# Kernel optimization log

Measured on AMD Instinct MI355X. Metric: run time of the kernel, lower is better.

## Reference

```python
import jax, jax.numpy as jnp
import numpy as np

N, M, E = 128, 256, 64
S, B = 1024, 512


def setup_inputs() -> dict:
    key = jax.random.key(0)
    ks = jax.random.split(key, 8)
    context = jax.random.normal(ks[0], (S, B, N), dtype=jnp.float32)
    z = jax.random.normal(ks[1], (M, B), dtype=jnp.float32)
    noise = jax.random.normal(ks[2], (N, B), dtype=jnp.float32)
    # parameters (match torch init semantics)
    conv_w = jax.random.normal(ks[3], (N, N, 2), dtype=jnp.float32) * (1.0 / np.sqrt(N * 2))
    conv_b = jnp.zeros((N,), dtype=jnp.float32)
    D = jnp.zeros((N, M), dtype=jnp.float32).at[:, :N].set(jnp.eye(N, dtype=jnp.float32))
    sigma = jnp.ones((N,), dtype=jnp.float32) * 0.05
    temp1 = jnp.array([0.1], dtype=jnp.float32)
    temp2 = jnp.array([0.1], dtype=jnp.float32)
    W1 = jax.random.normal(ks[4], (E, M + N), dtype=jnp.float32) * (1.0 / np.sqrt(M + N))
    b1 = jnp.zeros((E,), dtype=jnp.float32)
    W2 = jax.random.normal(ks[5], (E, E), dtype=jnp.float32) * (1.0 / np.sqrt(E))
    b2 = jnp.zeros((E,), dtype=jnp.float32)
    return {"context": context, "z": z, "noise": noise, "conv_w": conv_w,
            "conv_b": conv_b, "D": D, "sigma": sigma, "temp1": temp1,
            "W1": W1, "b1": b1, "W2": W2, "b2": b2, "temp2": temp2}


def reference(context, z, noise, conv_w, conv_b, D, sigma, temp1, W1, b1, W2, b2, temp2):
    # z_obs = D @ detach(z)  -> [N, B]
    z_obs = D @ jax.lax.stop_gradient(z)
    z_current = z_obs + sigma[:, None] * noise            # [N, B]
    z_current_t = z_current.T                             # [B, N]
    # L1 distance attention over the first S-1 frames
    distances = jnp.sum(jnp.abs(context[:-1] - z_current_t[None]), axis=2)  # [S-1, B]
    attn = jax.nn.softmax(-distances / jnp.abs(temp1[0]), axis=0)           # [S-1, B]
    # conv1d over seq axis: x [B, N, S], w [N_out, N_in, 2], valid padding -> [B, N, S-1]
    x = jnp.transpose(context, (1, 2, 0))
    enc = jax.lax.conv_general_dilated(x, conv_w, window_strides=(1,), padding='VALID',
                                       dimension_numbers=('NCH', 'OIH', 'NCH'))
    enc = enc + conv_b[None, :, None]
    encoded = jnp.transpose(enc, (2, 0, 1))               # [S-1, B, N]
    # attention-weighted sum over frames
    embedding = jnp.einsum('sbn,sb->nb', encoded, attn)   # [N, B]
    combined_t = jnp.concatenate([embedding, z], axis=0).T  # [B, N+M]
    h = jax.nn.relu(combined_t @ W1.T + b1)
    mlp_out = h @ W2.T + b2                               # [B, E]
    w_exp = jax.nn.softmax(-mlp_out.T / jnp.abs(temp2[0]), axis=0)  # [E, B]
    return w_exp
```

## Files before the change

kernel.cpp:

```cpp
#include <hip/hip_runtime.h>
#include <math.h>

#define Bq 512
#define Nq 128
#define Mq 256
#define Eq 64
#define SM1 1023
#define LOG2E 1.4426950408889634f

__device__ __forceinline__ float waveReduceSumAll(float x) {
    x += __int_as_float(__builtin_amdgcn_update_dpp(0, __float_as_int(x), 0x111, 0xf, 0xf, true));
    x += __int_as_float(__builtin_amdgcn_update_dpp(0, __float_as_int(x), 0x112, 0xf, 0xf, true));
    x += __int_as_float(__builtin_amdgcn_update_dpp(0, __float_as_int(x), 0x114, 0xf, 0xf, true));
    x += __int_as_float(__builtin_amdgcn_update_dpp(0, __float_as_int(x), 0x118, 0xf, 0xf, true));
    x += __int_as_float(__builtin_amdgcn_update_dpp(0, __float_as_int(x), 0x142, 0xf, 0xf, true));
    x += __int_as_float(__builtin_amdgcn_update_dpp(0, __float_as_int(x), 0x143, 0xf, 0xf, true));
    return __int_as_float(__builtin_amdgcn_readlane(__float_as_int(x), 63));
}

#define ROW_BODY(K, RK, DOLOAD)                                          \
    {                                                                    \
        float2 c  = buf[(K)];                                            \
        float2 cn = buf[((K) + 1) & 7];                                  \
        if (DOLOAD) buf[(K)] = p2[(size_t)min((RK) + 8, hi) * 32768];    \
        float d = fabsf(c.x - zcx) + fabsf(c.y - zcy);                   \
        d = waveReduceSumAll(d);                                         \
        float v = d * negt;                    \
        float mnew = fmaxf(mrun, v);                                     \
        float sc = exp2f(mrun - mnew);           \
        float w  = exp2f(v - mnew);                                      \
        mrun = mnew;                                                     \
        Zrun = fmaf(Zrun, sc, w);                                        \
        a0x = fmaf(a0x, sc, w * c.x);                                    \
        a0y = fmaf(a0y, sc, w * c.y);                                    \
        a1x = fmaf(a1x, sc, w * cn.x);                                   \
        a1y = fmaf(a1y, sc, w * cn.y);                                   \
    }

extern "C" __global__ void __launch_bounds__(512, 4)
gating_kernel(const float* __restrict__ context,
              const float* __restrict__ z,
              const float* __restrict__ noise,
              const float* __restrict__ conv_w,
              const float* __restrict__ conv_b,
              const float* __restrict__ D,
              const float* __restrict__ sigma,
              const float* __restrict__ temp1,
              const float* __restrict__ W1,
              const float* __restrict__ b1,
              const float* __restrict__ W2,
              const float* __restrict__ b2,
              const float* __restrict__ temp2,
              float* __restrict__ out)
{
    const int b    = blockIdx.x;
    const int tid  = threadIdx.x;
    const int wave = tid >> 6;
    const int lane = tid & 63;

    __shared__ __align__(16) float sA0[8][128];
    __shared__ __align__(16) float sA1[8][128];
    __shared__ float smx[8];
    __shared__ float sZ[8];
    __shared__ __align__(16) float gA0[128];
    __shared__ __align__(16) float gA1[128];
    __shared__ __align__(16) float semb[128];
    __shared__ __align__(16) float szc[128];
    __shared__ __align__(16) float szcol[256];
    __shared__ __align__(16) float shb[64];

    const int lo = wave * 128;
    const int hi = min(SM1, lo + 128);
    const float2* p2 = (const float2*)context + (size_t)b * 64 + lane;

    float2 buf[8];
    #pragma unroll
    for (int j = 0; j < 8; ++j)
        buf[j] = p2[(size_t)min(lo + j, hi) * 32768];

    if (tid < 256) szcol[tid] = z[tid * Bq + b];
    __syncthreads();
    if (tid < 128) {
        const float4* Drow = (const float4*)(D + tid * Mq);
        float acc0 = 0.f, acc1 = 0.f, acc2 = 0.f, acc3 = 0.f;
        #pragma unroll 8
        for (int i = 0; i < 64; ++i) {
            float4 dv = Drow[i];
            acc0 = fmaf(dv.x, szcol[4 * i + 0], acc0);
            acc1 = fmaf(dv.y, szcol[4 * i + 1], acc1);
            acc2 = fmaf(dv.z, szcol[4 * i + 2], acc2);
            acc3 = fmaf(dv.w, szcol[4 * i + 3], acc3);
        }
        szc[tid] = (acc0 + acc1) + (acc2 + acc3) + sigma[tid] * noise[tid * Bq + b];
    }
    __syncthreads();

    const float negt = -LOG2E / fabsf(temp1[0]);
    const float zcx = szc[2 * lane];
    const float zcy = szc[2 * lane + 1];

    float mrun = -INFINITY, Zrun = 0.f;
    float a0x = 0.f, a0y = 0.f, a1x = 0.f, a1y = 0.f;

    int r = lo;
    for (; r + 8 <= hi; r += 8) {
        #pragma unroll
        for (int k = 0; k < 8; ++k)
            ROW_BODY(k, r + k, 1)
    }
    #pragma unroll
    for (int j = 0; j < 7; ++j) {
        if (r + j < hi)
            ROW_BODY(j, r + j, 0)
    }

    *(float2*)&sA0[wave][2 * lane] = make_float2(a0x, a0y);
    *(float2*)&sA1[wave][2 * lane] = make_float2(a1x, a1y);
    if (lane == 0) { smx[wave] = mrun; sZ[wave] = Zrun; }
    __syncthreads();

    float gm = smx[0];
    #pragma unroll
    for (int k = 1; k < 8; ++k) gm = fmaxf(gm, smx[k]);
    float scl[8];
    float Gz = 0.f;
    #pragma unroll
    for (int k = 0; k < 8; ++k) { scl[k] = exp2f(smx[k] - gm); Gz = fmaf(scl[k], sZ[k], Gz); }

    if (tid < 128) {
        float acc = 0.f;
        #pragma unroll
        for (int k = 0; k < 8; ++k) acc = fmaf(scl[k], sA0[k][tid], acc);
        gA0[tid] = acc;
    } else if (tid < 256) {
        const int t = tid - 128;
        float acc = 0.f;
        #pragma unroll
        for (int k = 0; k < 8; ++k) acc = fmaf(scl[k], sA1[k][t], acc);
        gA1[t] = acc;
    }
    __syncthreads();

    if (tid < 128) {
        const float4* wr = (const float4*)(conv_w + tid * 256);
        float acc = 0.f;
        #pragma unroll 8
        for (int i = 0; i < 64; ++i) {
            float4 w4 = wr[i];
            acc = fmaf(w4.x, gA0[2 * i], acc);
            acc = fmaf(w4.y, gA1[2 * i], acc);
            acc = fmaf(w4.z, gA0[2 * i + 1], acc);
            acc = fmaf(w4.w, gA1[2 * i + 1], acc);
        }
        semb[tid] = acc / Gz + conv_b[tid];
    }
    __syncthreads();

    if (tid < 64) {
        const float* w1r = W1 + tid * (Nq + Mq);
        float acc = b1[tid];
        #pragma unroll 8
        for (int i = 0; i < 128; ++i) acc = fmaf(w1r[i], semb[i], acc);
        #pragma unroll 8
        for (int i = 0; i < 256; ++i) acc = fmaf(w1r[128 + i], szcol[i], acc);
        shb[tid] = fmaxf(acc, 0.f);
    }
    __syncthreads();

    if (tid < 64) {
        const float* w2r = W2 + tid * Eq;
        float acc = b2[tid];
        #pragma unroll 8
        for (int j = 0; j < 64; ++j) acc = fmaf(w2r[j], shb[j], acc);
        float v = -acc * (LOG2E / fabsf(temp2[0]));
        float mx = v;
        #pragma unroll
        for (int off = 32; off > 0; off >>= 1) mx = fmaxf(mx, __shfl_xor(mx, off, 64));
        float w = exp2f(v - mx);
        float s = w;
        #pragma unroll
        for (int off = 32; off > 0; off >>= 1) s += __shfl_xor(s, off, 64);
        out[tid * Bq + b] = w / s;
    }
}

extern "C" void kernel_launch(void* const* d_in, const int* in_sizes, int n_in,
                              void* d_out, int out_size, void* d_ws, size_t ws_size,
                              hipStream_t stream) {
    const float* context = (const float*)d_in[0];
    const float* z       = (const float*)d_in[1];
    const float* noise   = (const float*)d_in[2];
    const float* conv_w  = (const float*)d_in[3];
    const float* conv_b  = (const float*)d_in[4];
    const float* D       = (const float*)d_in[5];
    const float* sigma   = (const float*)d_in[6];
    const float* temp1   = (const float*)d_in[7];
    const float* W1      = (const float*)d_in[8];
    const float* b1      = (const float*)d_in[9];
    const float* W2      = (const float*)d_in[10];
    const float* b2      = (const float*)d_in[11];
    const float* temp2   = (const float*)d_in[12];
    float* out = (float*)d_out;

    gating_kernel<<<dim3(Bq), dim3(512), 0, stream>>>(
        context, z, noise, conv_w, conv_b, D, sigma, temp1,
        W1, b1, W2, b2, temp2, out);
}
```

Baseline: 69.87 us.

## Split gating kernel into zc, sequence-split streaming, and merge kernels

Splits the single fused kernel into three launches. A small kernel computes z_current for all columns. A streaming kernel runs 1024 blocks, each handling two batch columns over a quarter of the sequence: half-waves, float4 loads and 16-deep register prefetch, writing partial online-softmax results to workspace. A merge kernel combines the four partials and runs the conv/MLP/softmax tail with vectorized W1 loads. The aim is more parallelism and wider memory accesses on the 268MB context stream, at the cost of extra launches and workspace traffic.

New measurement: 128.0 us. +83.2%, slower.

```diff
diff --git a/kernel.cpp b/kernel.cpp
--- a/kernel.cpp
+++ b/kernel.cpp
@@ -8,141 +8,198 @@
 #define SM1 1023
 #define LOG2E 1.4426950408889634f
 
-__device__ __forceinline__ float waveReduceSumAll(float x) {
-    x += __int_as_float(__builtin_amdgcn_update_dpp(0, __float_as_int(x), 0x111, 0xf, 0xf, true));
-    x += __int_as_float(__builtin_amdgcn_update_dpp(0, __float_as_int(x), 0x112, 0xf, 0xf, true));
-    x += __int_as_float(__builtin_amdgcn_update_dpp(0, __float_as_int(x), 0x114, 0xf, 0xf, true));
-    x += __int_as_float(__builtin_amdgcn_update_dpp(0, __float_as_int(x), 0x118, 0xf, 0xf, true));
-    x += __int_as_float(__builtin_amdgcn_update_dpp(0, __float_as_int(x), 0x142, 0xf, 0xf, true));
-    x += __int_as_float(__builtin_amdgcn_update_dpp(0, __float_as_int(x), 0x143, 0xf, 0xf, true));
-    return __int_as_float(__builtin_amdgcn_readlane(__float_as_int(x), 63));
-}
-
-#define ROW_BODY(K, RK, DOLOAD)                                          \
+#define WS_ZC 0
+#define WS_A0 65536
+#define WS_A1 327680
+#define WS_MZ 589824
+
+__device__ __forceinline__ float halfReduce32(float x) {
+    x += __int_as_float(__builtin_amdgcn_update_dpp(0, __float_as_int(x), 0x0B1, 0xf, 0xf, true));
+    x += __int_as_float(__builtin_amdgcn_update_dpp(0, __float_as_int(x), 0x04E, 0xf, 0xf, true));
+    x += __int_as_float(__builtin_amdgcn_update_dpp(0, __float_as_int(x), 0x141, 0xf, 0xf, true));
+    x += __int_as_float(__builtin_amdgcn_update_dpp(0, __float_as_int(x), 0x140, 0xf, 0xf, true));
+    x += __int_as_float(__builtin_amdgcn_ds_swizzle(__float_as_int(x), 0x401F));
+    return x;
+}
+
+extern "C" __global__ void __launch_bounds__(512)
+zc_kernel(const float* __restrict__ z, const float* __restrict__ noise,
+          const float* __restrict__ D, const float* __restrict__ sigma,
+          float* __restrict__ ws)
+{
+    const int b4 = blockIdx.x * 4;
+    const int t  = threadIdx.x;
+    __shared__ float zs[4][256];
+    for (int i = t; i < 1024; i += 512)
+        zs[i >> 8][i & 255] = z[(i & 255) * Bq + b4 + (i >> 8)];
+    __syncthreads();
+    const int c = t >> 7, o = t & 127;
+    const float4* Dr = (const float4*)(D + o * Mq);
+    const float* zc = zs[c];
+    float a0 = 0.f, a1 = 0.f, a2 = 0.f, a3 = 0.f;
+    #pragma unroll 8
+    for (int i = 0; i < 64; ++i) {
+        float4 dv = Dr[i];
+        a0 = fmaf(dv.x, zc[4 * i + 0], a0);
+        a1 = fmaf(dv.y, zc[4 * i + 1], a1);
+        a2 = fmaf(dv.z, zc[4 * i + 2], a2);
+        a3 = fmaf(dv.w, zc[4 * i + 3], a3);
+    }
+    ws[WS_ZC + (b4 + c) * Nq + o] =
+        (a0 + a1) + (a2 + a3) + sigma[o] * noise[o * Bq + b4 + c];
+}
+
+#define ROW_BODY(K, RK, DOREFILL, CN)                                    \
     {                                                                    \
-        float2 c  = buf[(K)];                                            \
-        float2 cn = buf[((K) + 1) & 7];                                  \
-        if (DOLOAD) buf[(K)] = p2[(size_t)min((RK) + 8, hi) * 32768];    \
-        float d = fabsf(c.x - zcx) + fabsf(c.y - zcy);                   \
-        d = waveReduceSumAll(d);                                         \
-        float v = d * negt;                    \
+        float4 c  = buf[(K)];                                            \
+        float4 cn = (CN);                                                \
+        if (DOREFILL) buf[(K)] = p4[(size_t)((RK) + 16) * 16384];        \
+        float d = (fabsf(c.x - zcv.x) + fabsf(c.y - zcv.y)) +            \
+                  (fabsf(c.z - zcv.z) + fabsf(c.w - zcv.w));             \
+        d = halfReduce32(d);                                             \
+        float v = d * negt;                                              \
         float mnew = fmaxf(mrun, v);                                     \
-        float sc = exp2f(mrun - mnew);           \
+        float sc = exp2f(mrun - mnew);                                   \
         float w  = exp2f(v - mnew);                                      \
         mrun = mnew;                                                     \
         Zrun = fmaf(Zrun, sc, w);                                        \
-        a0x = fmaf(a0x, sc, w * c.x);                                    \
-        a0y = fmaf(a0y, sc, w * c.y);                                    \
-        a1x = fmaf(a1x, sc, w * cn.x);                                   \
-        a1y = fmaf(a1y, sc, w * cn.y);                                   \
-    }
-
-extern "C" __global__ void __launch_bounds__(512, 4)
-gating_kernel(const float* __restrict__ context,
-              const float* __restrict__ z,
-              const float* __restrict__ noise,
-              const float* __restrict__ conv_w,
-              const float* __restrict__ conv_b,
-              const float* __restrict__ D,
-              const float* __restrict__ sigma,
+        a0.x = fmaf(a0.x, sc, w * c.x);                                  \
+        a0.y = fmaf(a0.y, sc, w * c.y);                                  \
+        a0.z = fmaf(a0.z, sc, w * c.z);                                  \
+        a0.w = fmaf(a0.w, sc, w * c.w);                                  \
+        a1.x = fmaf(a1.x, sc, w * cn.x);                                 \
+        a1.y = fmaf(a1.y, sc, w * cn.y);                                 \
+        a1.z = fmaf(a1.z, sc, w * cn.z);                                 \
+        a1.w = fmaf(a1.w, sc, w * cn.w);                                 \
+    }
+
+extern "C" __global__ void __launch_bounds__(512, 8)
+stream_kernel(const float* __restrict__ context,
               const float* __restrict__ temp1,
-              const float* __restrict__ W1,
-              const float* __restrict__ b1,
-              const float* __restrict__ W2,
-              const float* __restrict__ b2,
-              const float* __restrict__ temp2,
-              float* __restrict__ out)
+              float* __restrict__ ws)
 {
-    const int b    = blockIdx.x;
     const int tid  = threadIdx.x;
     const int wave = tid >> 6;
     const int lane = tid & 63;
-
-    __shared__ __align__(16) float sA0[8][128];
-    __shared__ __align__(16) float sA1[8][128];
-    __shared__ float smx[8];
-    __shared__ float sZ[8];
+    const int half = lane >> 5;
+    const int l5   = lane & 31;
+    const int q    = blockIdx.x & 3;
+    const int b0   = (blockIdx.x >> 2) * 2;
+
+    __shared__ __align__(16) float sA0[8][2][128];
+    __shared__ __align__(16) float sA1[8][2][128];
+    __shared__ float sM[8][2];
+    __shared__ float sZw[8][2];
+
+    const int lo = q * 256 + wave * 32;
+    const int hi = min(SM1, lo + 32);
+
+    const float4* p4 = (const float4*)context + (size_t)b0 * 32 + lane;
+
+    float4 buf[16];
+    #pragma unroll
+    for (int j = 0; j < 16; ++j)
+        buf[j] = p4[(size_t)(lo + j) * 16384];
+    float4 cextra = p4[(size_t)hi * 16384];
+
+    const float4 zcv = *(const float4*)(ws + WS_ZC + (size_t)(b0 + half) * Nq + l5 * 4);
+    const float negt = -LOG2E / fabsf(temp1[0]);
+
+    float mrun = -INFINITY, Zrun = 0.f;
+    float4 a0 = make_float4(0.f, 0.f, 0.f, 0.f);
+    float4 a1 = make_float4(0.f, 0.f, 0.f, 0.f);
+
+    #pragma unroll
+    for (int k = 0; k < 16; ++k)
+        ROW_BODY(k, lo + k, 1, buf[(k + 1) & 15])
+    #pragma unroll
+    for (int j = 0; j < 15; ++j) {
+        if (lo + 16 + j < hi)
+            ROW_BODY(j, lo + 16 + j, 0, buf[j + 1])
+    }
+    if (lo + 31 < hi)
+        ROW_BODY(15, lo + 31, 0, cextra)
+
+    *(float4*)&sA0[wave][half][l5 * 4] = a0;
+    *(float4*)&sA1[wave][half][l5 * 4] = a1;
+    if (l5 == 0) { sM[wave][half] = mrun; sZw[wave][half] = Zrun; }
+    __syncthreads();
+
+    const int c = (tid >> 7) & 1;
+    const int o = tid & 127;
+    float gm = sM[0][c];
+    #pragma unroll
+    for (int w = 1; w < 8; ++w) gm = fmaxf(gm, sM[w][c]);
+    float scl[8];
+    float Gz = 0.f;
+    #pragma unroll
+    for (int w = 0; w < 8; ++w) { scl[w] = exp2f(sM[w][c] - gm); Gz = fmaf(scl[w], sZw[w][c], Gz); }
+
+    const size_t pslot = (size_t)q * Bq + b0 + c;
+    if (tid < 256) {
+        float acc = 0.f;
+        #pragma unroll
+        for (int w = 0; w < 8; ++w) acc = fmaf(scl[w], sA0[w][c][o], acc);
+        ws[WS_A0 + pslot * Nq + o] = acc;
+        if (o == 0) {
+            ws[WS_MZ + pslot * 2]     = gm;
+            ws[WS_MZ + pslot * 2 + 1] = Gz;
+        }
+    } else {
+        float acc = 0.f;
+        #pragma unroll
+        for (int w = 0; w < 8; ++w) acc = fmaf(scl[w], sA1[w][c][o], acc);
+        ws[WS_A1 + pslot * Nq + o] = acc;
+    }
+}
+
+extern "C" __global__ void __launch_bounds__(128)
+merge_kernel(const float* __restrict__ ws,
+             const float* __restrict__ z,
+             const float* __restrict__ conv_w,
+             const float* __restrict__ conv_b,
+             const float* __restrict__ W1,
+             const float* __restrict__ b1,
+             const float* __restrict__ W2,
+             const float* __restrict__ b2,
+             const float* __restrict__ temp2,
+             float* __restrict__ out)
+{
+    const int col = blockIdx.x;
+    const int t   = threadIdx.x;
     __shared__ __align__(16) float gA0[128];
     __shared__ __align__(16) float gA1[128];
     __shared__ __align__(16) float semb[128];
-    __shared__ __align__(16) float szc[128];
     __shared__ __align__(16) float szcol[256];
     __shared__ __align__(16) float shb[64];
 
-    const int lo = wave * 128;
-    const int hi = min(SM1, lo + 128);
-    const float2* p2 = (const float2*)context + (size_t)b * 64 + lane;
-
-    float2 buf[8];
-    #pragma unroll
-    for (int j = 0; j < 8; ++j)
-        buf[j] = p2[(size_t)min(lo + j, hi) * 32768];
-
-    if (tid < 256) szcol[tid] = z[tid * Bq + b];
-    __syncthreads();
-    if (tid < 128) {
-        const float4* Drow = (const float4*)(D + tid * Mq);
-        float acc0 = 0.f, acc1 = 0.f, acc2 = 0.f, acc3 = 0.f;
-        #pragma unroll 8
-        for (int i = 0; i < 64; ++i) {
-            float4 dv = Drow[i];
-            acc0 = fmaf(dv.x, szcol[4 * i + 0], acc0);
-            acc1 = fmaf(dv.y, szcol[4 * i + 1], acc1);
-            acc2 = fmaf(dv.z, szcol[4 * i + 2], acc2);
-            acc3 = fmaf(dv.w, szcol[4 * i + 3], acc3);
-        }
-        szc[tid] = (acc0 + acc1) + (acc2 + acc3) + sigma[tid] * noise[tid * Bq + b];
-    }
-    __syncthreads();
-
-    const float negt = -LOG2E / fabsf(temp1[0]);
-    const float zcx = szc[2 * lane];
-    const float zcy = szc[2 * lane + 1];
-
-    float mrun = -INFINITY, Zrun = 0.f;
-    float a0x = 0.f, a0y = 0.f, a1x = 0.f, a1y = 0.f;
-
-    int r = lo;
-    for (; r + 8 <= hi; r += 8) {
-        #pragma unroll
-        for (int k = 0; k < 8; ++k)
-            ROW_BODY(k, r + k, 1)
-    }
-    #pragma unroll
-    for (int j = 0; j < 7; ++j) {
-        if (r + j < hi)
-            ROW_BODY(j, r + j, 0)
-    }
-
-    *(float2*)&sA0[wave][2 * lane] = make_float2(a0x, a0y);
-    *(float2*)&sA1[wave][2 * lane] = make_float2(a1x, a1y);
-    if (lane == 0) { smx[wave] = mrun; sZ[wave] = Zrun; }
-    __syncthreads();
-
-    float gm = smx[0];
-    #pragma unroll
-    for (int k = 1; k < 8; ++k) gm = fmaxf(gm, smx[k]);
-    float scl[8];
+    szcol[t]       = z[t * Bq + col];
+    szcol[t + 128] = z[(t + 128) * Bq + col];
+
+    float m[4], Zp[4];
+    #pragma unroll
+    for (int p = 0; p < 4; ++p) {
+        m[p]  = ws[WS_MZ + ((size_t)p * Bq + col) * 2];
+        Zp[p] = ws[WS_MZ + ((size_t)p * Bq + col) * 2 + 1];
+    }
+    float gm = fmaxf(fmaxf(m[0], m[1]), fmaxf(m[2], m[3]));
     float Gz = 0.f;
-    #pragma unroll
-    for (int k = 0; k < 8; ++k) { scl[k] = exp2f(smx[k] - gm); Gz = fmaf(scl[k], sZ[k], Gz); }
-
-    if (tid < 128) {
-        float acc = 0.f;
-        #pragma unroll
-        for (int k = 0; k < 8; ++k) acc = fmaf(scl[k], sA0[k][tid], acc);
-        gA0[tid] = acc;
-    } else if (tid < 256) {
-        const int t = tid - 128;
-        float acc = 0.f;
-        #pragma unroll
-        for (int k = 0; k < 8; ++k) acc = fmaf(scl[k], sA1[k][t], acc);
-        gA1[t] = acc;
-    }
-    __syncthreads();
-
-    if (tid < 128) {
-        const float4* wr = (const float4*)(conv_w + tid * 256);
+    float scl[4];
+    #pragma unroll
+    for (int p = 0; p < 4; ++p) { scl[p] = exp2f(m[p] - gm); Gz = fmaf(scl[p], Zp[p], Gz); }
+
+    float acc0 = 0.f, acc1 = 0.f;
+    #pragma unroll
+    for (int p = 0; p < 4; ++p) {
+        acc0 = fmaf(scl[p], ws[WS_A0 + ((size_t)p * Bq + col) * Nq + t], acc0);
+        acc1 = fmaf(scl[p], ws[WS_A1 + ((size_t)p * Bq + col) * Nq + t], acc1);
+    }
+    gA0[t] = acc0;
+    gA1[t] = acc1;
+    __syncthreads();
+
+    {
+        const float4* wr = (const float4*)(conv_w + t * 256);
         float acc = 0.f;
         #pragma unroll 8
         for (int i = 0; i < 64; ++i) {
@@ -152,24 +209,36 @@
             acc = fmaf(w4.z, gA0[2 * i + 1], acc);
             acc = fmaf(w4.w, gA1[2 * i + 1], acc);
         }
-        semb[tid] = acc / Gz + conv_b[tid];
-    }
-    __syncthreads();
-
-    if (tid < 64) {
-        const float* w1r = W1 + tid * (Nq + Mq);
-        float acc = b1[tid];
-        #pragma unroll 8
-        for (int i = 0; i < 128; ++i) acc = fmaf(w1r[i], semb[i], acc);
-        #pragma unroll 8
-        for (int i = 0; i < 256; ++i) acc = fmaf(w1r[128 + i], szcol[i], acc);
-        shb[tid] = fmaxf(acc, 0.f);
-    }
-    __syncthreads();
-
-    if (tid < 64) {
-        const float* w2r = W2 + tid * Eq;
-        float acc = b2[tid];
+        semb[t] = acc / Gz + conv_b[t];
+    }
+    __syncthreads();
+
+    if (t < 64) {
+        const float4* w1r = (const float4*)(W1 + t * (Nq + Mq));
+        float acc = b1[t];
+        #pragma unroll 8
+        for (int i = 0; i < 32; ++i) {
+            float4 wv = w1r[i];
+            acc = fmaf(wv.x, semb[4 * i + 0], acc);
+            acc = fmaf(wv.y, semb[4 * i + 1], acc);
+            acc = fmaf(wv.z, semb[4 * i + 2], acc);
+            acc = fmaf(wv.w, semb[4 * i + 3], acc);
+        }
+        #pragma unroll 8
+        for (int i = 0; i < 64; ++i) {
+            float4 wv = w1r[32 + i];
+            acc = fmaf(wv.x, szcol[4 * i + 0], acc);
+            acc = fmaf(wv.y, szcol[4 * i + 1], acc);
+            acc = fmaf(wv.z, szcol[4 * i + 2], acc);
+            acc = fmaf(wv.w, szcol[4 * i + 3], acc);
+        }
+        shb[t] = fmaxf(acc, 0.f);
+    }
+    __syncthreads();
+
+    if (t < 64) {
+        const float* w2r = W2 + t * Eq;
+        float acc = b2[t];
         #pragma unroll 8
         for (int j = 0; j < 64; ++j) acc = fmaf(w2r[j], shb[j], acc);
         float v = -acc * (LOG2E / fabsf(temp2[0]));
@@ -180,7 +249,7 @@
         float s = w;
         #pragma unroll
         for (int off = 32; off > 0; off >>= 1) s += __shfl_xor(s, off, 64);
-        out[tid * Bq + b] = w / s;
+        out[t * Bq + col] = w / s;
     }
 }
 
@@ -201,8 +270,10 @@
     const float* b2      = (const float*)d_in[11];
     const float* temp2   = (const float*)d_in[12];
     float* out = (float*)d_out;
-
-    gating_kernel<<<dim3(Bq), dim3(512), 0, stream>>>(
-        context, z, noise, conv_w, conv_b, D, sigma, temp1,
-        W1, b1, W2, b2, temp2, out);
-}
+    float* ws  = (float*)d_ws;
+
+    zc_kernel<<<dim3(128), dim3(512), 0, stream>>>(z, noise, D, sigma, ws);
+    stream_kernel<<<dim3(1024), dim3(512), 0, stream>>>(context, temp1, ws);
+    merge_kernel<<<dim3(512), dim3(128), 0, stream>>>(ws, z, conv_w, conv_b,
+                                                      W1, b1, W2, b2, temp2, out);
+}
```

## Split streaming pass across two blocks per column and move MLP to epilogue kernel

Applied to the files above, without the earlier changes.

The single fused kernel becomes two. A streaming kernel uses two blocks per batch column, each covering half the sequence and writing partial online-softmax state (max, normaliser, accumulators) to workspace. A separate epilogue kernel merges the halves and runs the conv projection and MLP for four columns per block. The conv neighbour term now reuses the previous row's weight instead of loading a second row, and launch bounds rise to 8 blocks per CU. This adds parallelism and occupancy for the bandwidth-bound context scan, at the cost of a second launch and a workspace round trip.

Measured after the change: 97.06 us. 1.39x slower.

```diff
diff --git a/kernel.cpp b/kernel.cpp
--- a/kernel.cpp
+++ b/kernel.cpp
@@ -5,8 +5,9 @@
 #define Nq 128
 #define Mq 256
 #define Eq 64
-#define SM1 1023
 #define LOG2E 1.4426950408889634f
+
+#define PSTRIDE 264
 
 __device__ __forceinline__ float waveReduceSumAll(float x) {
     x += __int_as_float(__builtin_amdgcn_update_dpp(0, __float_as_int(x), 0x111, 0xf, 0xf, true));
@@ -18,101 +19,95 @@
     return __int_as_float(__builtin_amdgcn_readlane(__float_as_int(x), 63));
 }
 
-#define ROW_BODY(K, RK, DOLOAD)                                          \
+#define ROWB(K, S, RF)                                                   \
     {                                                                    \
-        float2 c  = buf[(K)];                                            \
-        float2 cn = buf[((K) + 1) & 7];                                  \
-        if (DOLOAD) buf[(K)] = p2[(size_t)min((RK) + 8, hi) * 32768];    \
-        float d = fabsf(c.x - zcx) + fabsf(c.y - zcy);                   \
+        float2 e = buf[(K)];                                             \
+        if (RF) buf[(K)] = p2[(size_t)((S) + 8) * 32768];                \
+        float d = fabsf(e.x - zcx) + fabsf(e.y - zcy);                   \
         d = waveReduceSumAll(d);                                         \
-        float v = d * negt;                    \
+        float v = d * negt;                                              \
         float mnew = fmaxf(mrun, v);                                     \
-        float sc = exp2f(mrun - mnew);           \
+        float sc = exp2f(mrun - mnew);                                   \
         float w  = exp2f(v - mnew);                                      \
+        float wp = wprev * sc;                                           \
         mrun = mnew;                                                     \
         Zrun = fmaf(Zrun, sc, w);                                        \
-        a0x = fmaf(a0x, sc, w * c.x);                                    \
-        a0y = fmaf(a0y, sc, w * c.y);                                    \
-        a1x = fmaf(a1x, sc, w * cn.x);                                   \
-        a1y = fmaf(a1y, sc, w * cn.y);                                   \
-    }
-
-extern "C" __global__ void __launch_bounds__(512, 4)
-gating_kernel(const float* __restrict__ context,
+        a0x = fmaf(a0x, sc, w * e.x);                                    \
+        a0y = fmaf(a0y, sc, w * e.y);                                    \
+        a1x = fmaf(a1x, sc, wp * e.x);                                   \
+        a1y = fmaf(a1y, sc, wp * e.y);                                   \
+        wprev = w;                                                       \
+    }
+
+extern "C" __global__ void __launch_bounds__(512, 8)
+stream_kernel(const float* __restrict__ context,
               const float* __restrict__ z,
               const float* __restrict__ noise,
-              const float* __restrict__ conv_w,
-              const float* __restrict__ conv_b,
               const float* __restrict__ D,
               const float* __restrict__ sigma,
               const float* __restrict__ temp1,
-              const float* __restrict__ W1,
-              const float* __restrict__ b1,
-              const float* __restrict__ W2,
-              const float* __restrict__ b2,
-              const float* __restrict__ temp2,
-              float* __restrict__ out)
+              float* __restrict__ ws)
 {
-    const int b    = blockIdx.x;
     const int tid  = threadIdx.x;
     const int wave = tid >> 6;
     const int lane = tid & 63;
+    const int col  = blockIdx.x >> 1;
+    const int half = blockIdx.x & 1;
 
     __shared__ __align__(16) float sA0[8][128];
     __shared__ __align__(16) float sA1[8][128];
     __shared__ float smx[8];
     __shared__ float sZ[8];
-    __shared__ __align__(16) float gA0[128];
-    __shared__ __align__(16) float gA1[128];
-    __shared__ __align__(16) float semb[128];
     __shared__ __align__(16) float szc[128];
     __shared__ __align__(16) float szcol[256];
-    __shared__ __align__(16) float shb[64];
-
-    const int lo = wave * 128;
-    const int hi = min(SM1, lo + 128);
-    const float2* p2 = (const float2*)context + (size_t)b * 64 + lane;
+
+    const int lo = half * 512 + wave * 64;
+    const int hi = min(1023, lo + 64);
+
+    const float2* p2 = (const float2*)context + (size_t)col * 64 + lane;
 
     float2 buf[8];
     #pragma unroll
     for (int j = 0; j < 8; ++j)
-        buf[j] = p2[(size_t)min(lo + j, hi) * 32768];
-
-    if (tid < 256) szcol[tid] = z[tid * Bq + b];
+        buf[j] = p2[(size_t)(lo + j) * 32768];
+    float2 xtra = p2[(size_t)hi * 32768];
+
+    if (tid < 256) szcol[tid] = z[tid * Bq + col];
     __syncthreads();
     if (tid < 128) {
         const float4* Drow = (const float4*)(D + tid * Mq);
-        float acc0 = 0.f, acc1 = 0.f, acc2 = 0.f, acc3 = 0.f;
+        float c0 = 0.f, c1 = 0.f, c2 = 0.f, c3 = 0.f;
         #pragma unroll 8
         for (int i = 0; i < 64; ++i) {
             float4 dv = Drow[i];
-            acc0 = fmaf(dv.x, szcol[4 * i + 0], acc0);
-            acc1 = fmaf(dv.y, szcol[4 * i + 1], acc1);
-            acc2 = fmaf(dv.z, szcol[4 * i + 2], acc2);
-            acc3 = fmaf(dv.w, szcol[4 * i + 3], acc3);
-        }
-        szc[tid] = (acc0 + acc1) + (acc2 + acc3) + sigma[tid] * noise[tid * Bq + b];
-    }
-    __syncthreads();
-
-    const float negt = -LOG2E / fabsf(temp1[0]);
+            c0 = fmaf(dv.x, szcol[4 * i + 0], c0);
+            c1 = fmaf(dv.y, szcol[4 * i + 1], c1);
+            c2 = fmaf(dv.z, szcol[4 * i + 2], c2);
+            c3 = fmaf(dv.w, szcol[4 * i + 3], c3);
+        }
+        szc[tid] = (c0 + c1) + (c2 + c3) + sigma[tid] * noise[tid * Bq + col];
+    }
+    __syncthreads();
+
     const float zcx = szc[2 * lane];
     const float zcy = szc[2 * lane + 1];
-
-    float mrun = -INFINITY, Zrun = 0.f;
+    const float negt = -LOG2E / fabsf(temp1[0]);
+
+    float mrun = -INFINITY, Zrun = 0.f, wprev = 0.f;
     float a0x = 0.f, a0y = 0.f, a1x = 0.f, a1y = 0.f;
 
-    int r = lo;
-    for (; r + 8 <= hi; r += 8) {
-        #pragma unroll
-        for (int k = 0; k < 8; ++k)
-            ROW_BODY(k, r + k, 1)
-    }
-    #pragma unroll
-    for (int j = 0; j < 7; ++j) {
-        if (r + j < hi)
-            ROW_BODY(j, r + j, 0)
-    }
+    int rb = lo;
+    for (; rb + 8 < hi; rb += 8) {
+        ROWB(0, rb+0, 1) ROWB(1, rb+1, 1) ROWB(2, rb+2, 1) ROWB(3, rb+3, 1)
+        ROWB(4, rb+4, 1) ROWB(5, rb+5, 1) ROWB(6, rb+6, 1) ROWB(7, rb+7, 1)
+    }
+    #pragma unroll
+    for (int j = 0; j < 8; ++j) {
+        if (rb + j < hi)
+            ROWB(j, rb + j, 0)
+    }
+    a1x = fmaf(wprev, xtra.x, a1x);
+    a1y = fmaf(wprev, xtra.y, a1y);
 
     *(float2*)&sA0[wave][2 * lane] = make_float2(a0x, a0y);
     *(float2*)&sA1[wave][2 * lane] = make_float2(a1x, a1y);
@@ -127,51 +122,105 @@
     #pragma unroll
     for (int k = 0; k < 8; ++k) { scl[k] = exp2f(smx[k] - gm); Gz = fmaf(scl[k], sZ[k], Gz); }
 
+    float* pb = ws + (size_t)(col * 2 + half) * PSTRIDE;
     if (tid < 128) {
         float acc = 0.f;
         #pragma unroll
         for (int k = 0; k < 8; ++k) acc = fmaf(scl[k], sA0[k][tid], acc);
-        gA0[tid] = acc;
+        pb[tid] = acc;
     } else if (tid < 256) {
         const int t = tid - 128;
         float acc = 0.f;
         #pragma unroll
         for (int k = 0; k < 8; ++k) acc = fmaf(scl[k], sA1[k][t], acc);
-        gA1[t] = acc;
-    }
-    __syncthreads();
-
-    if (tid < 128) {
-        const float4* wr = (const float4*)(conv_w + tid * 256);
+        pb[128 + t] = acc;
+    } else if (tid == 256) {
+        pb[256] = gm;
+        pb[257] = Gz;
+    }
+}
+
+extern "C" __global__ void __launch_bounds__(512)
+epilogue_kernel(const float* __restrict__ ws,
+                const float* __restrict__ z,
+                const float* __restrict__ conv_w,
+                const float* __restrict__ conv_b,
+                const float* __restrict__ W1,
+                const float* __restrict__ b1,
+                const float* __restrict__ W2,
+                const float* __restrict__ b2,
+                const float* __restrict__ temp2,
+                float* __restrict__ out)
+{
+    const int t   = threadIdx.x;
+    const int cs  = t >> 7;
+    const int o   = t & 127;
+    const int col = blockIdx.x * 4 + cs;
+
+    __shared__ __align__(16) float gA0[4][128];
+    __shared__ __align__(16) float gA1[4][128];
+    __shared__ __align__(16) float semb[4][128];
+    __shared__ __align__(16) float szcol[4][256];
+    __shared__ __align__(16) float shb[4][64];
+
+    szcol[cs][o]       = z[o * Bq + col];
+    szcol[cs][o + 128] = z[(o + 128) * Bq + col];
+
+    const float* P0 = ws + (size_t)(col * 2 + 0) * PSTRIDE;
+    const float* P1 = ws + (size_t)(col * 2 + 1) * PSTRIDE;
+    const float m0 = P0[256], Z0 = P0[257];
+    const float m1 = P1[256], Z1 = P1[257];
+    const float gm = fmaxf(m0, m1);
+    const float s0 = exp2f(m0 - gm), s1 = exp2f(m1 - gm);
+    const float Gz = fmaf(s0, Z0, s1 * Z1);
+
+    gA0[cs][o] = fmaf(s0, P0[o],       s1 * P1[o]);
+    gA1[cs][o] = fmaf(s0, P0[128 + o], s1 * P1[128 + o]);
+    __syncthreads();
+
+    {
+        const float4* wr = (const float4*)(conv_w + o * 256);
         float acc = 0.f;
         #pragma unroll 8
         for (int i = 0; i < 64; ++i) {
             float4 w4 = wr[i];
-            acc = fmaf(w4.x, gA0[2 * i], acc);
-            acc = fmaf(w4.y, gA1[2 * i], acc);
-            acc = fmaf(w4.z, gA0[2 * i + 1], acc);
-            acc = fmaf(w4.w, gA1[2 * i + 1], acc);
-        }
-        semb[tid] = acc / Gz + conv_b[tid];
-    }
-    __syncthreads();
-
-    if (tid < 64) {
-        const float* w1r = W1 + tid * (Nq + Mq);
-        float acc = b1[tid];
-        #pragma unroll 8
-        for (int i = 0; i < 128; ++i) acc = fmaf(w1r[i], semb[i], acc);
-        #pragma unroll 8
-        for (int i = 0; i < 256; ++i) acc = fmaf(w1r[128 + i], szcol[i], acc);
-        shb[tid] = fmaxf(acc, 0.f);
-    }
-    __syncthreads();
-
-    if (tid < 64) {
-        const float* w2r = W2 + tid * Eq;
-        float acc = b2[tid];
-        #pragma unroll 8
-        for (int j = 0; j < 64; ++j) acc = fmaf(w2r[j], shb[j], acc);
+            acc = fmaf(w4.x, gA0[cs][2 * i], acc);
+            acc = fmaf(w4.y, gA1[cs][2 * i], acc);
+            acc = fmaf(w4.z, gA0[cs][2 * i + 1], acc);
+            acc = fmaf(w4.w, gA1[cs][2 * i + 1], acc);
+        }
+        semb[cs][o] = acc / Gz + conv_b[o];
+    }
+    __syncthreads();
+
+    if (o < 64) {
+        const float4* w1r = (const float4*)(W1 + o * (Nq + Mq));
+        float acc = b1[o];
+        #pragma unroll 8
+        for (int i = 0; i < 32; ++i) {
+            float4 wv = w1r[i];
+            acc = fmaf(wv.x, semb[cs][4 * i + 0], acc);
+            acc = fmaf(wv.y, semb[cs][4 * i + 1], acc);
+            acc = fmaf(wv.z, semb[cs][4 * i + 2], acc);
+            acc = fmaf(wv.w, semb[cs][4 * i + 3], acc);
+        }
+        #pragma unroll 8
+        for (int i = 0; i < 64; ++i) {
+            float4 wv = w1r[32 + i];
+            acc = fmaf(wv.x, szcol[cs][4 * i + 0], acc);
+            acc = fmaf(wv.y, szcol[cs][4 * i + 1], acc);
+            acc = fmaf(wv.z, szcol[cs][4 * i + 2], acc);
+            acc = fmaf(wv.w, szcol[cs][4 * i + 3], acc);
+        }
+        shb[cs][o] = fmaxf(acc, 0.f);
+    }
+    __syncthreads();
+
+    if (o < 64) {
+        const float* w2r = W2 + o * Eq;
+        float acc = b2[o];
+        #pragma unroll 8
+        for (int jj = 0; jj < 64; ++jj) acc = fmaf(w2r[jj], shb[cs][jj], acc);
         float v = -acc * (LOG2E / fabsf(temp2[0]));
         float mx = v;
         #pragma unroll
@@ -180,7 +229,7 @@
         float s = w;
         #pragma unroll
         for (int off = 32; off > 0; off >>= 1) s += __shfl_xor(s, off, 64);
-        out[tid * Bq + b] = w / s;
+        out[o * Bq + col] = w / s;
     }
 }
 
@@ -201,8 +250,10 @@
     const float* b2      = (const float*)d_in[11];
     const float* temp2   = (const float*)d_in[12];
     float* out = (float*)d_out;
-
-    gating_kernel<<<dim3(Bq), dim3(512), 0, stream>>>(
-        context, z, noise, conv_w, conv_b, D, sigma, temp1,
-        W1, b1, W2, b2, temp2, out);
-}
+    float* ws  = (float*)d_ws;
+
+    stream_kernel<<<dim3(1024), dim3(512), 0, stream>>>(
+        context, z, noise, D, sigma, temp1, ws);
+    epilogue_kernel<<<dim3(128), dim3(512), 0, stream>>>(
+        ws, z, conv_w, conv_b, W1, b1, W2, b2, temp2, out);
+}
```

## Split each wave into two half-wave row streams with float4 loads

Applied to the files above, without the earlier changes.

Each wave now processes two independent row ranges, one per 32-lane half. Each lane loads a float4 instead of a float2, and the L1 distance is reduced with a 32-lane DPP plus swizzle reduction instead of a full-wave reduction with readlane. The next-row term of the conv is now carried as the previous row's weight, so one load per row serves both taps instead of two buffered reads. This aims to halve the reduction depth and double row-level parallelism per wave. In exchange it needs 16 partial accumulators in shared memory and an extra tail load per half-wave.

After: 67.41 us, median of 2. -3.5%, faster.

```diff
diff --git a/kernel.cpp b/kernel.cpp
--- a/kernel.cpp
+++ b/kernel.cpp
@@ -5,36 +5,39 @@
 #define Nq 128
 #define Mq 256
 #define Eq 64
-#define SM1 1023
 #define LOG2E 1.4426950408889634f
 
-__device__ __forceinline__ float waveReduceSumAll(float x) {
-    x += __int_as_float(__builtin_amdgcn_update_dpp(0, __float_as_int(x), 0x111, 0xf, 0xf, true));
-    x += __int_as_float(__builtin_amdgcn_update_dpp(0, __float_as_int(x), 0x112, 0xf, 0xf, true));
-    x += __int_as_float(__builtin_amdgcn_update_dpp(0, __float_as_int(x), 0x114, 0xf, 0xf, true));
-    x += __int_as_float(__builtin_amdgcn_update_dpp(0, __float_as_int(x), 0x118, 0xf, 0xf, true));
-    x += __int_as_float(__builtin_amdgcn_update_dpp(0, __float_as_int(x), 0x142, 0xf, 0xf, true));
-    x += __int_as_float(__builtin_amdgcn_update_dpp(0, __float_as_int(x), 0x143, 0xf, 0xf, true));
-    return __int_as_float(__builtin_amdgcn_readlane(__float_as_int(x), 63));
+#define DPPADD(X, CTRL) \
+    (X) += __int_as_float(__builtin_amdgcn_update_dpp(0, __float_as_int(X), (CTRL), 0xf, 0xf, true));
+
+__device__ __forceinline__ float halfReduce32(float x) {
+    DPPADD(x, 0x0B1)
+    DPPADD(x, 0x04E)
+    DPPADD(x, 0x141)
+    DPPADD(x, 0x140)
+    x += __int_as_float(__builtin_amdgcn_ds_swizzle(__float_as_int(x), 0x401F));
+    return x;
 }
 
-#define ROW_BODY(K, RK, DOLOAD)                                          \
-    {                                                                    \
-        float2 c  = buf[(K)];                                            \
-        float2 cn = buf[((K) + 1) & 7];                                  \
-        if (DOLOAD) buf[(K)] = p2[(size_t)min((RK) + 8, hi) * 32768];    \
-        float d = fabsf(c.x - zcx) + fabsf(c.y - zcy);                   \
-        d = waveReduceSumAll(d);                                         \
-        float v = d * negt;                    \
-        float mnew = fmaxf(mrun, v);                                     \
-        float sc = exp2f(mrun - mnew);           \
-        float w  = exp2f(v - mnew);                                      \
-        mrun = mnew;                                                     \
-        Zrun = fmaf(Zrun, sc, w);                                        \
-        a0x = fmaf(a0x, sc, w * c.x);                                    \
-        a0y = fmaf(a0y, sc, w * c.y);                                    \
-        a1x = fmaf(a1x, sc, w * cn.x);                                   \
-        a1y = fmaf(a1y, sc, w * cn.y);                                   \
+#define ROWB(K, S, RF)                                                    \
+    {                                                                     \
+        float4 e = buf[(K)];                                              \
+        if (RF) buf[(K)] = pr[(size_t)((S) + 8) * 16384];                 \
+        float d = (fabsf(e.x - zc0.x) + fabsf(e.y - zc0.y)) +             \
+                  (fabsf(e.z - zc0.z) + fabsf(e.w - zc0.w));              \
+        d = halfReduce32(d);                                              \
+        float v = d * negt;                                               \
+        float mnew = fmaxf(mrun, v);                                      \
+        float sc = exp2f(mrun - mnew);                                    \
+        float w  = exp2f(v - mnew);                                       \
+        float wp = wprev * sc;                                            \
+        mrun = mnew;                                                      \
+        Zrun = fmaf(Zrun, sc, w);                                         \
+        a0.x = fmaf(a0.x, sc, w * e.x);   a0.y = fmaf(a0.y, sc, w * e.y); \
+        a0.z = fmaf(a0.z, sc, w * e.z);   a0.w = fmaf(a0.w, sc, w * e.w); \
+        a1.x = fmaf(a1.x, sc, wp * e.x);  a1.y = fmaf(a1.y, sc, wp * e.y);\
+        a1.z = fmaf(a1.z, sc, wp * e.z);  a1.w = fmaf(a1.w, sc, wp * e.w);\
+        wprev = w;                                                        \
     }
 
 extern "C" __global__ void __launch_bounds__(512, 4)
@@ -57,11 +60,14 @@
     const int tid  = threadIdx.x;
     const int wave = tid >> 6;
     const int lane = tid & 63;
-
-    __shared__ __align__(16) float sA0[8][128];
-    __shared__ __align__(16) float sA1[8][128];
-    __shared__ float smx[8];
-    __shared__ float sZ[8];
+    const int half = lane >> 5;
+    const int l5   = lane & 31;
+    const int idx  = wave * 2 + half;
+
+    __shared__ __align__(16) float sA0[16][128];
+    __shared__ __align__(16) float sA1[16][128];
+    __shared__ float smx[16];
+    __shared__ float sZ[16];
     __shared__ __align__(16) float gA0[128];
     __shared__ __align__(16) float gA1[128];
     __shared__ __align__(16) float semb[128];
@@ -69,74 +75,77 @@
     __shared__ __align__(16) float szcol[256];
     __shared__ __align__(16) float shb[64];
 
-    const int lo = wave * 128;
-    const int hi = min(SM1, lo + 128);
-    const float2* p2 = (const float2*)context + (size_t)b * 64 + lane;
-
-    float2 buf[8];
+    const int myLo = wave * 128 + half * 64;
+    const int myHi = min(1023, myLo + 64);
+
+    const float4* pr = (const float4*)context + (size_t)b * 32 + l5;
+
+    float4 buf[8];
     #pragma unroll
     for (int j = 0; j < 8; ++j)
-        buf[j] = p2[(size_t)min(lo + j, hi) * 32768];
+        buf[j] = pr[(size_t)(myLo + j) * 16384];
+    float4 xtra = pr[(size_t)myHi * 16384];
 
     if (tid < 256) szcol[tid] = z[tid * Bq + b];
     __syncthreads();
     if (tid < 128) {
         const float4* Drow = (const float4*)(D + tid * Mq);
-        float acc0 = 0.f, acc1 = 0.f, acc2 = 0.f, acc3 = 0.f;
+        float c0 = 0.f, c1 = 0.f, c2 = 0.f, c3 = 0.f;
         #pragma unroll 8
         for (int i = 0; i < 64; ++i) {
             float4 dv = Drow[i];
-            acc0 = fmaf(dv.x, szcol[4 * i + 0], acc0);
-            acc1 = fmaf(dv.y, szcol[4 * i + 1], acc1);
-            acc2 = fmaf(dv.z, szcol[4 * i + 2], acc2);
-            acc3 = fmaf(dv.w, szcol[4 * i + 3], acc3);
+            c0 = fmaf(dv.x, szcol[4 * i + 0], c0);
+            c1 = fmaf(dv.y, szcol[4 * i + 1], c1);
+            c2 = fmaf(dv.z, szcol[4 * i + 2], c2);
+            c3 = fmaf(dv.w, szcol[4 * i + 3], c3);
         }
-        szc[tid] = (acc0 + acc1) + (acc2 + acc3) + sigma[tid] * noise[tid * Bq + b];
-    }
-    __syncthreads();
-
+        szc[tid] = (c0 + c1) + (c2 + c3) + sigma[tid] * noise[tid * Bq + b];
+    }
+    __syncthreads();
+
+    const float4 zc0 = *(const float4*)&szc[l5 * 4];
     const float negt = -LOG2E / fabsf(temp1[0]);
-    const float zcx = szc[2 * lane];
-    const float zcy = szc[2 * lane + 1];
-
-    float mrun = -INFINITY, Zrun = 0.f;
-    float a0x = 0.f, a0y = 0.f, a1x = 0.f, a1y = 0.f;
-
-    int r = lo;
-    for (; r + 8 <= hi; r += 8) {
-        #pragma unroll
-        for (int k = 0; k < 8; ++k)
-            ROW_BODY(k, r + k, 1)
-    }
-    #pragma unroll
-    for (int j = 0; j < 7; ++j) {
-        if (r + j < hi)
-            ROW_BODY(j, r + j, 0)
-    }
-
-    *(float2*)&sA0[wave][2 * lane] = make_float2(a0x, a0y);
-    *(float2*)&sA1[wave][2 * lane] = make_float2(a1x, a1y);
-    if (lane == 0) { smx[wave] = mrun; sZ[wave] = Zrun; }
+
+    float mrun = -INFINITY, Zrun = 0.f, wprev = 0.f;
+    float4 a0 = make_float4(0.f, 0.f, 0.f, 0.f);
+    float4 a1 = make_float4(0.f, 0.f, 0.f, 0.f);
+
+    int rb = myLo;
+    for (; rb + 8 < myHi; rb += 8) {
+        ROWB(0, rb+0, 1) ROWB(1, rb+1, 1) ROWB(2, rb+2, 1) ROWB(3, rb+3, 1)
+        ROWB(4, rb+4, 1) ROWB(5, rb+5, 1) ROWB(6, rb+6, 1) ROWB(7, rb+7, 1)
+    }
+    #pragma unroll
+    for (int j = 0; j < 8; ++j) {
+        if (rb + j < myHi)
+            ROWB(j, rb + j, 0)
+    }
+    a1.x = fmaf(wprev, xtra.x, a1.x); a1.y = fmaf(wprev, xtra.y, a1.y);
+    a1.z = fmaf(wprev, xtra.z, a1.z); a1.w = fmaf(wprev, xtra.w, a1.w);
+
+    *(float4*)&sA0[idx][l5 * 4] = a0;
+    *(float4*)&sA1[idx][l5 * 4] = a1;
+    if (l5 == 0) { smx[idx] = mrun; sZ[idx] = Zrun; }
     __syncthreads();
 
     float gm = smx[0];
     #pragma unroll
-    for (int k = 1; k < 8; ++k) gm = fmaxf(gm, smx[k]);
-    float scl[8];
+    for (int k = 1; k < 16; ++k) gm = fmaxf(gm, smx[k]);
+    float scl[16];
     float Gz = 0.f;
     #pragma unroll
-    for (int k = 0; k < 8; ++k) { scl[k] = exp2f(smx[k] - gm); Gz = fmaf(scl[k], sZ[k], Gz); }
+    for (int k = 0; k < 16; ++k) { scl[k] = exp2f(smx[k] - gm); Gz = fmaf(scl[k], sZ[k], Gz); }
 
     if (tid < 128) {
         float acc = 0.f;
         #pragma unroll
-        for (int k = 0; k < 8; ++k) acc = fmaf(scl[k], sA0[k][tid], acc);
+        for (int k = 0; k < 16; ++k) acc = fmaf(scl[k], sA0[k][tid], acc);
         gA0[tid] = acc;
     } else if (tid < 256) {
         const int t = tid - 128;
         float acc = 0.f;
         #pragma unroll
-        for (int k = 0; k < 8; ++k) acc = fmaf(scl[k], sA1[k][t], acc);
+        for (int k = 0; k < 16; ++k) acc = fmaf(scl[k], sA1[k][t], acc);
         gA1[t] = acc;
     }
     __syncthreads();
```
